# Kernel tuning notes

Hardware: AMD Instinct MI355X
Metric: run time of the kernel (lower is better)

Reference implementation:

```python
import jax, jax.numpy as jnp
import numpy as np

B, T, D, H, L, F = 256, 32, 1024, 8, 3, 2048
SSRC, NCOL, NTAB, NACT, NSYM = 64, 32, 16, 64, 32
HD = D // H


def setup_inputs() -> dict:
    key = jax.random.key(0)
    ks = jax.random.split(key, 40)
    n = lambda k, s, sc=0.02: jax.random.normal(k, s, jnp.float32) * sc
    inp = {}
    inp["prev_action_emb"] = jax.random.normal(ks[0], (B, T, D), jnp.float32)
    inp["encoded_src"] = jax.random.normal(ks[1], (B, SSRC, D), jnp.float32)
    inp["encoded_col"] = jax.random.normal(ks[2], (B, NCOL, D), jnp.float32)
    inp["encoded_tab"] = jax.random.normal(ks[3], (B, NTAB, D), jnp.float32)
    inp["src_mask"] = jnp.zeros((B, SSRC), jnp.int32)  # 1 = padded
    inp["symbol_ids"] = jax.random.randint(ks[4], (B, T), 0, NSYM)
    inp["view_type"] = jax.random.randint(ks[5], (B,), 0, 3)  # 0=action,1=col,2=tab
    inp["gold_action"] = jax.random.randint(ks[6], (B,), 0, NACT)
    inp["gold_col"] = jax.random.randint(ks[7], (B,), 0, NCOL)
    inp["gold_tab"] = jax.random.randint(ks[8], (B,), 0, NTAB)
    # grammar embeddings (torch nn.Embedding default ~ N(0,1))
    inp["symbol_emb"] = jax.random.normal(ks[9], (NSYM, D), jnp.float32)
    inp["action_emb"] = jax.random.normal(ks[10], (NACT, D), jnp.float32)
    # affine heads
    inp["action_aff_w"] = n(ks[11], (D, D)); inp["action_aff_b"] = jnp.zeros((D,), jnp.float32)
    inp["symbol_aff_w"] = n(ks[12], (D, D)); inp["symbol_aff_b"] = jnp.zeros((D,), jnp.float32)
    inp["col_aff_w"] = n(ks[13], (D, D)); inp["col_aff_b"] = jnp.zeros((D,), jnp.float32)
    inp["tab_aff_w"] = n(ks[14], (D, D)); inp["tab_aff_b"] = jnp.zeros((D,), jnp.float32)
    inp["tgt_lin_w"] = n(ks[15], (2 * D, D)); inp["tgt_lin_b"] = jnp.zeros((D,), jnp.float32)
    inp["out_lin_w"] = n(ks[16], (D, D)); inp["out_lin_b"] = jnp.zeros((D,), jnp.float32)
    # transformer decoder layers (q,k,v,o stacked on axis 1)
    inp["self_w"] = n(ks[17], (L, 4, D, D)); inp["self_b"] = jnp.zeros((L, 4, D), jnp.float32)
    inp["cross_w"] = n(ks[18], (L, 4, D, D)); inp["cross_b"] = jnp.zeros((L, 4, D), jnp.float32)
    inp["ffn_w1"] = n(ks[19], (L, D, F)); inp["ffn_b1"] = jnp.zeros((L, F), jnp.float32)
    inp["ffn_w2"] = n(ks[20], (L, F, D)); inp["ffn_b2"] = jnp.zeros((L, D), jnp.float32)
    inp["ln_g"] = jnp.ones((L, 3, D), jnp.float32); inp["ln_b"] = jnp.zeros((L, 3, D), jnp.float32)
    return inp


def _pe(t, d):
    pos = jnp.arange(t, dtype=jnp.float32)[:, None]
    div = jnp.exp(jnp.arange(0, d, 2, dtype=jnp.float32) * (-np.log(10000.0) / d))
    pe = jnp.zeros((t, d), jnp.float32)
    pe = pe.at[:, 0::2].set(jnp.sin(pos * div)).at[:, 1::2].set(jnp.cos(pos * div))
    return pe


def _ln(x, g, b, eps=1e-5):
    m = jnp.mean(x, -1, keepdims=True)
    v = jnp.mean((x - m) ** 2, -1, keepdims=True)
    return (x - m) / jnp.sqrt(v + eps) * g + b


def _mha(xq, xkv, w, b, pad=None):
    # w: [4, D, D] for q,k,v,o; pad: [B, Tk] bool key-padding mask
    q = (xq @ w[0] + b[0]).reshape(xq.shape[0], -1, H, HD)
    k = (xkv @ w[1] + b[1]).reshape(xkv.shape[0], -1, H, HD)
    v = (xkv @ w[2] + b[2]).reshape(xkv.shape[0], -1, H, HD)
    s = jnp.einsum("bqhd,bkhd->bhqk", q, k) / np.sqrt(HD).astype(np.float32)
    if pad is not None:
        s = jnp.where(pad[:, None, None, :], -1e9, s)
    a = jax.nn.softmax(s, -1)
    o = jnp.einsum("bhqk,bkhd->bqhd", a, v).reshape(xq.shape[0], -1, D)
    return o @ w[3] + b[3]


def reference(prev_action_emb, encoded_src, encoded_col, encoded_tab, symbol_emb, action_emb,
              action_aff_w, action_aff_b, symbol_aff_w, symbol_aff_b, col_aff_w, col_aff_b,
              tab_aff_w, tab_aff_b, tgt_lin_w, tgt_lin_b, out_lin_w, out_lin_b,
              self_w, self_b, cross_w, cross_b, ffn_w1, ffn_b1, ffn_w2, ffn_b2, ln_g, ln_b,
              src_mask, symbol_ids, view_type, gold_action, gold_col, gold_tab):
    # target embeddings: affine(prev action emb) ++ affine(symbol emb gather)
    tgt_a = prev_action_emb @ action_aff_w + action_aff_b            # [B,T,D]
    tgt_s = symbol_emb[symbol_ids] @ symbol_aff_w + symbol_aff_b     # [B,T,D]
    x = jnp.concatenate([tgt_a, tgt_s], -1) @ tgt_lin_w + tgt_lin_b  # [B,T,D]
    x = x + _pe(T, D)[None]  # positional encoding (dropout = eval identity)
    pad = src_mask.astype(bool)
    for l in range(L):  # post-LN TransformerDecoderLayer (torch default, relu FFN)
        x = _ln(x + _mha(x, x, self_w[l], self_b[l]), ln_g[l, 0], ln_b[l, 0])
        x = _ln(x + _mha(x, encoded_src, cross_w[l], cross_b[l], pad), ln_g[l, 1], ln_b[l, 1])
        ff = jax.nn.relu(x @ ffn_w1[l] + ffn_b1[l]) @ ffn_w2[l] + ffn_b2[l]
        x = _ln(x + ff, ln_g[l, 2], ln_b[l, 2])
    out = x[:, -1, :] @ out_lin_w + out_lin_b  # [B,D], last decode position
    # three routed prediction heads: affine(src) . out -> masked log_softmax
    src_a = action_emb @ action_aff_w + action_aff_b                 # [A,D]
    logp_a = jax.nn.log_softmax(out @ src_a.T, -1)                   # [B,A]
    src_c = encoded_col @ col_aff_w + col_aff_b                      # [B,Nc,D]
    logp_c = jax.nn.log_softmax(jnp.einsum("bnd,bd->bn", src_c, out), -1)
    src_t = encoded_tab @ tab_aff_w + tab_aff_b                      # [B,Nt,D]
    logp_t = jax.nn.log_softmax(jnp.einsum("bnd,bd->bn", src_t, out), -1)
    ga = jnp.take_along_axis(logp_a, gold_action[:, None], 1)[:, 0]
    gc = jnp.take_along_axis(logp_c, gold_col[:, None], 1)[:, 0]
    gt = jnp.take_along_axis(logp_t, gold_tab[:, None], 1)[:, 0]
    # grammar routing: each example's loss comes from exactly one view
    nll = -jnp.where(view_type == 0, ga, jnp.where(view_type == 1, gc, gt))  # [B]
    return nll
```

## Files before the change

kernel.cpp:

```cpp
#include <hip/hip_runtime.h>

typedef float  f32x4 __attribute__((ext_vector_type(4)));
typedef short  s16x8 __attribute__((ext_vector_type(8)));

__device__ __forceinline__ float b2f(short s) {
    return __uint_as_float(((unsigned)(unsigned short)s) << 16);
}
__device__ __forceinline__ short f2b(float f) {
    unsigned u = __float_as_uint(f);
    u = u + 0x7fffu + ((u >> 16) & 1u);
    return (short)(u >> 16);
}

__device__ __forceinline__ void gld_lds16(const short* g, short* l) {
    __builtin_amdgcn_global_load_lds(
        (const __attribute__((address_space(1))) unsigned int*)(const void*)g,
        (__attribute__((address_space(3))) unsigned int*)(void*)l,
        16, 0, 0);
}

#define S_VMCNT(N)  asm volatile("s_waitcnt vmcnt(" #N ")" ::: "memory")
#define S_LGKM0     asm volatile("s_waitcnt lgkmcnt(0)" ::: "memory")
#define SBAR        __builtin_amdgcn_s_barrier()
#define SCHED0      __builtin_amdgcn_sched_barrier(0)

template<int BM>
__global__ __launch_bounds__(512) void gemm_pipe(
    const short* __restrict__ A, const short* __restrict__ Bt,
    const float* __restrict__ bias,
    short* __restrict__ Cb,
    const short* __restrict__ res,
    const float* __restrict__ sym2, const int* __restrict__ sid,
    const float* __restrict__ pe,
    int M, int N, int K, int epi)
{
    constexpr int MF   = BM / 32;
    constexpr int ALW  = BM / 128;
    constexpr int BUFB = (BM + 256) * 64;
    __shared__ short lds[3 * BUFB / 2];

    const int tid  = threadIdx.x;
    const int lane = tid & 63;
    const int wave = tid >> 6;

    int bid = blockIdx.x;
    int nwg = gridDim.x;
    if ((nwg & 7) == 0) { int q = nwg >> 3; bid = (bid & 7) * q + (bid >> 3); }
    const int nbx = N >> 8;
    const int m0 = (bid / nbx) * BM;
    const int n0 = (bid % nbx) * 256;

    const int wm = (wave >> 2) * (BM / 2);
    const int wn = (wave & 3) * 64;
    const int l15 = lane & 15, l4 = lane >> 4;

    f32x4 acc[MF][4];
#pragma unroll
    for (int m = 0; m < MF; m++)
#pragma unroll
        for (int n = 0; n < 4; n++)
#pragma unroll
            for (int j = 0; j < 4; j++) acc[m][n][j] = 0.f;

    int aoff[MF], boff[4];
#pragma unroll
    for (int m = 0; m < MF; m++) {
        int r = wm + m * 16 + l15;
        aoff[m] = r * 64 + ((l4 ^ ((r >> 1) & 3)) << 4);
    }
#pragma unroll
    for (int n = 0; n < 4; n++) {
        int r = wn + n * 16 + l15;
        boff[n] = BM * 64 + r * 64 + ((l4 ^ ((r >> 1) & 3)) << 4);
    }

    size_t agoff[ALW]; int aldo[ALW];
#pragma unroll
    for (int i = 0; i < ALW; i++) {
        int rr = (wave * ALW + i) * 16 + (lane >> 2);
        int c  = (lane & 3) ^ ((rr >> 1) & 3);
        agoff[i] = (size_t)(m0 + rr) * K + c * 8;
        aldo[i]  = (wave * ALW + i) * 1024;
    }
    size_t bgoff[2]; int bldo[2];
#pragma unroll
    for (int i = 0; i < 2; i++) {
        int rr = (wave * 2 + i) * 16 + (lane >> 2);
        int c  = (lane & 3) ^ ((rr >> 1) & 3);
        bgoff[i] = (size_t)(n0 + rr) * K + c * 8;
        bldo[i]  = BM * 64 + (wave * 2 + i) * 1024;
    }

    char* lbase = (char*)lds;
    auto stage = [&](int kt, int bufoff) {
        char* lb = lbase + bufoff;
#pragma unroll
        for (int i = 0; i < ALW; i++)
            gld_lds16(A + agoff[i] + (size_t)kt * 32, (short*)(lb + aldo[i]));
#pragma unroll
        for (int i = 0; i < 2; i++)
            gld_lds16(Bt + bgoff[i] + (size_t)kt * 32, (short*)(lb + bldo[i]));
    };

    const int NT = K >> 5;
    stage(0, 0);
    stage(1, BUFB);
    if constexpr (BM == 256) S_VMCNT(4); else S_VMCNT(3);
    SBAR; SCHED0;

    int cbo = 0, sbo = 2 * BUFB;
    for (int t = 0; t < NT; t++) {
        if (t + 2 < NT) stage(t + 2, sbo);
        if constexpr (BM == 256) S_VMCNT(8); else S_VMCNT(6);
        SCHED0;
        s16x8 af[MF], bfv[4];
        const char* cp = lbase + cbo;
#pragma unroll
        for (int m = 0; m < MF; m++) af[m]  = *(const s16x8*)(cp + aoff[m]);
#pragma unroll
        for (int n = 0; n < 4; n++)  bfv[n] = *(const s16x8*)(cp + boff[n]);
        S_LGKM0;
        SCHED0;
        if constexpr (BM == 256) S_VMCNT(4); else S_VMCNT(3);
        SBAR; SCHED0;
        __builtin_amdgcn_s_setprio(1);
#pragma unroll
        for (int m = 0; m < MF; m++)
#pragma unroll
            for (int n = 0; n < 4; n++)
                acc[m][n] = __builtin_amdgcn_mfma_f32_16x16x32_bf16(
                    af[m], bfv[n], acc[m][n], 0, 0, 0);
        __builtin_amdgcn_s_setprio(0);
        cbo += BUFB; if (cbo == 3 * BUFB) cbo = 0;
        sbo += BUFB; if (sbo == 3 * BUFB) sbo = 0;
    }

#pragma unroll
    for (int m = 0; m < MF; m++) {
#pragma unroll
        for (int n = 0; n < 4; n++) {
#pragma unroll
            for (int j = 0; j < 4; j++) {
                int row = m0 + wm + m * 16 + l4 * 4 + j;
                int col = n0 + wn + n * 16 + l15;
                float v = acc[m][n][j];
                if (bias) v += bias[col];
                size_t idx = (size_t)row * N + col;
                if (epi == 0) {
                    Cb[idx] = f2b(v);
                } else if (epi == 2) {
                    v += sym2[(size_t)sid[row] * 1024 + col] + pe[(size_t)(row & 31) * 1024 + col];
                    Cb[idx] = f2b(v);
                } else if (epi == 3) {
                    Cb[idx] = f2b(fmaxf(v, 0.f));
                } else {
                    Cb[idx] = f2b(v + b2f(res[idx]));
                }
            }
        }
    }
}

__global__ __launch_bounds__(256) void gemm_bt(
    const short* __restrict__ A, const short* __restrict__ Bt,
    const float* __restrict__ bias,
    float* __restrict__ Cf, short* __restrict__ Cb,
    const short* __restrict__ res,
    int M, int N, int K, int epi)
{
    __shared__ short As[128 * 64];
    __shared__ short Bs[128 * 64];
    const int tid  = threadIdx.x;
    const int lane = tid & 63;
    const int wave = tid >> 6;
    const int m0 = blockIdx.y * 128, n0 = blockIdx.x * 128;
    const int wm = (wave >> 1) * 64, wn = (wave & 1) * 64;
    const int l15 = lane & 15, l4 = lane >> 4;

    f32x4 acc[4][4];
#pragma unroll
    for (int m = 0; m < 4; m++)
#pragma unroll
        for (int n = 0; n < 4; n++)
#pragma unroll
            for (int j = 0; j < 4; j++) acc[m][n][j] = 0.f;

    const int srow = wave * 32 + (lane >> 3);
    const int scol = (lane & 7) * 8;
    const short* Ag = A  + (size_t)(m0 + srow) * K + scol;
    const short* Bg = Bt + (size_t)(n0 + srow) * K + scol;
    short* Al = As + (wave * 32) * 64;
    short* Bl = Bs + (wave * 32) * 64;

    for (int k0 = 0; k0 < K; k0 += 64) {
#pragma unroll
        for (int i = 0; i < 4; i++) {
            gld_lds16(Ag + (size_t)(i * 8) * K + k0, Al + i * 8 * 64);
            gld_lds16(Bg + (size_t)(i * 8) * K + k0, Bl + i * 8 * 64);
        }
        __syncthreads();
#pragma unroll
        for (int kk = 0; kk < 64; kk += 32) {
            s16x8 af[4], bfv[4];
#pragma unroll
            for (int m = 0; m < 4; m++)
                af[m] = *(const s16x8*)(As + (wm + m * 16 + l15) * 64 + kk + l4 * 8);
#pragma unroll
            for (int n = 0; n < 4; n++)
                bfv[n] = *(const s16x8*)(Bs + (wn + n * 16 + l15) * 64 + kk + l4 * 8);
#pragma unroll
            for (int m = 0; m < 4; m++)
#pragma unroll
                for (int n = 0; n < 4; n++)
                    acc[m][n] = __builtin_amdgcn_mfma_f32_16x16x32_bf16(
                        af[m], bfv[n], acc[m][n], 0, 0, 0);
        }
        __syncthreads();
    }

#pragma unroll
    for (int m = 0; m < 4; m++) {
#pragma unroll
        for (int n = 0; n < 4; n++) {
#pragma unroll
            for (int j = 0; j < 4; j++) {
                int row = m0 + wm + m * 16 + l4 * 4 + j;
                int col = n0 + wn + n * 16 + l15;
                float v = acc[m][n][j];
                if (bias) v += bias[col];
                size_t idx = (size_t)row * N + col;
                if (epi == 0) {
                    Cb[idx] = f2b(v);
                } else if (epi == 1) {
                    Cf[idx] = v;
                } else if (epi == 3) {
                    Cb[idx] = f2b(fmaxf(v, 0.f));
                } else if (epi == 6) {
                    Cb[idx] = f2b(v + b2f(res[idx]));
                } else {
                    Cf[idx] = v; Cb[idx] = f2b(v);
                }
            }
        }
    }
}

__global__ __launch_bounds__(256) void attn_self(const short* __restrict__ qkv,
                                                 short* __restrict__ o)
{
    const int b = blockIdx.x >> 3, h = blockIdx.x & 7;
    __shared__ short Q[32 * 128], Kk[32 * 128], Vv[32 * 128];
    __shared__ float S[32 * 32];
    const int tid = threadIdx.x;
    const size_t base = (size_t)b * 32 * 3072 + h * 128;
    for (int i = tid; i < 512; i += 256) {
        int r = i >> 4, c = (i & 15) * 8;
        size_t g = base + (size_t)r * 3072 + c;
        *(s16x8*)(Q  + r * 128 + c) = *(const s16x8*)(qkv + g);
        *(s16x8*)(Kk + r * 128 + c) = *(const s16x8*)(qkv + g + 1024);
        *(s16x8*)(Vv + r * 128 + c) = *(const s16x8*)(qkv + g + 2048);
    }
    __syncthreads();
    for (int i = tid; i < 1024; i += 256) {
        int r = i >> 5, c = i & 31;
        float s = 0.f;
        for (int d8 = 0; d8 < 16; d8++) {
            s16x8 qa = *(const s16x8*)(Q  + r * 128 + d8 * 8);
            s16x8 ka = *(const s16x8*)(Kk + c * 128 + d8 * 8);
#pragma unroll
            for (int j = 0; j < 8; j++) s += b2f(qa[j]) * b2f(ka[j]);
        }
        S[i] = s * 0.088388347648318447f;
    }
    __syncthreads();
    if (tid < 32) {
        float mx = -1e30f;
        for (int c = 0; c < 32; c++) mx = fmaxf(mx, S[tid * 32 + c]);
        float sum = 0.f;
        for (int c = 0; c < 32; c++) { float p = __expf(S[tid * 32 + c] - mx); S[tid * 32 + c] = p; sum += p; }
        float inv = 1.f / sum;
        for (int c = 0; c < 32; c++) S[tid * 32 + c] *= inv;
    }
    __syncthreads();
    for (int i = tid; i < 4096; i += 256) {
        int r = i >> 7, d = i & 127;
        float a = 0.f;
        for (int c = 0; c < 32; c++) a += S[r * 32 + c] * b2f(Vv[c * 128 + d]);
        o[(size_t)(b * 32 + r) * 1024 + h * 128 + d] = f2b(a);
    }
}

__global__ __launch_bounds__(256) void attn_cross(const short* __restrict__ q_,
                                                  const short* __restrict__ ckv,
                                                  const int* __restrict__ mask,
                                                  short* __restrict__ o)
{
    const int b = blockIdx.x >> 3, h = blockIdx.x & 7;
    __shared__ short Q[32 * 128], Kk[64 * 128], Vv[64 * 128];
    __shared__ float S[32 * 64];
    const int tid = threadIdx.x;
    for (int i = tid; i < 512; i += 256) {
        int r = i >> 4, c = (i & 15) * 8;
        *(s16x8*)(Q + r * 128 + c) = *(const s16x8*)(q_ + (size_t)(b * 32 + r) * 1024 + h * 128 + c);
    }
    for (int i = tid; i < 1024; i += 256) {
        int r = i >> 4, c = (i & 15) * 8;
        size_t g = (size_t)(b * 64 + r) * 2048 + h * 128 + c;
        *(s16x8*)(Kk + r * 128 + c) = *(const s16x8*)(ckv + g);
        *(s16x8*)(Vv + r * 128 + c) = *(const s16x8*)(ckv + g + 1024);
    }
    __syncthreads();
    for (int i = tid; i < 2048; i += 256) {
        int r = i >> 6, c = i & 63;
        float s = 0.f;
        for (int d8 = 0; d8 < 16; d8++) {
            s16x8 qa = *(const s16x8*)(Q  + r * 128 + d8 * 8);
            s16x8 ka = *(const s16x8*)(Kk + c * 128 + d8 * 8);
#pragma unroll
            for (int j = 0; j < 8; j++) s += b2f(qa[j]) * b2f(ka[j]);
        }
        s *= 0.088388347648318447f;
        if (mask[b * 64 + c] != 0) s = -1e9f;
        S[i] = s;
    }
    __syncthreads();
    if (tid < 32) {
        float mx = -1e30f;
        for (int c = 0; c < 64; c++) mx = fmaxf(mx, S[tid * 64 + c]);
        float sum = 0.f;
        for (int c = 0; c < 64; c++) { float p = __expf(S[tid * 64 + c] - mx); S[tid * 64 + c] = p; sum += p; }
        float inv = 1.f / sum;
        for (int c = 0; c < 64; c++) S[tid * 64 + c] *= inv;
    }
    __syncthreads();
    for (int i = tid; i < 4096; i += 256) {
        int r = i >> 7, d = i & 127;
        float a = 0.f;
        for (int c = 0; c < 64; c++) a += S[r * 64 + c] * b2f(Vv[c * 128 + d]);
        o[(size_t)(b * 32 + r) * 1024 + h * 128 + d] = f2b(a);
    }
}

__global__ __launch_bounds__(256) void attn_self_last(const short* __restrict__ q,
                                                      const short* __restrict__ kv,
                                                      short* __restrict__ out)
{
    __shared__ float qs[4][128];
    __shared__ float ps[4][32];
    const int wave = threadIdx.x >> 6, lane = threadIdx.x & 63;
    const int idx = blockIdx.x * 4 + wave;
    const int b = idx >> 3, h = idx & 7;
    for (int d = lane; d < 128; d += 64)
        qs[wave][d] = b2f(q[(size_t)b * 1024 + h * 128 + d]);
    __syncthreads();
    float s = -1e30f;
    if (lane < 32) {
        const short* kr = kv + (size_t)(b * 32 + lane) * 2048 + h * 128;
        float a = 0.f;
        for (int d = 0; d < 128; d += 8) {
            s16x8 kvv = *(const s16x8*)(kr + d);
#pragma unroll
            for (int j = 0; j < 8; j++) a += qs[wave][d + j] * b2f(kvv[j]);
        }
        s = a * 0.088388347648318447f;
    }
    float mx = s;
#pragma unroll
    for (int o = 1; o < 32; o <<= 1) mx = fmaxf(mx, __shfl_xor(mx, o));
    float p = (lane < 32) ? __expf(s - mx) : 0.f;
    float sum = p;
#pragma unroll
    for (int o = 1; o < 32; o <<= 1) sum += __shfl_xor(sum, o);
    if (lane < 32) ps[wave][lane] = p / sum;
    __syncthreads();
    for (int d = lane; d < 128; d += 64) {
        float a = 0.f;
        for (int j = 0; j < 32; j++)
            a += ps[wave][j] * b2f(kv[(size_t)(b * 32 + j) * 2048 + 1024 + h * 128 + d]);
        out[(size_t)b * 1024 + h * 128 + d] = f2b(a);
    }
}

__global__ __launch_bounds__(256) void attn_cross_last(const short* __restrict__ q,
                                                       const short* __restrict__ ckv,
                                                       const int* __restrict__ mask,
                                                       short* __restrict__ out)
{
    __shared__ float qs[4][128];
    __shared__ float ps[4][64];
    const int wave = threadIdx.x >> 6, lane = threadIdx.x & 63;
    const int idx = blockIdx.x * 4 + wave;
    const int b = idx >> 3, h = idx & 7;
    for (int d = lane; d < 128; d += 64)
        qs[wave][d] = b2f(q[(size_t)b * 1024 + h * 128 + d]);
    __syncthreads();
    const short* kr = ckv + (size_t)(b * 64 + lane) * 2048 + h * 128;
    float a = 0.f;
    for (int d = 0; d < 128; d += 8) {
        s16x8 kvv = *(const s16x8*)(kr + d);
#pragma unroll
        for (int j = 0; j < 8; j++) a += qs[wave][d + j] * b2f(kvv[j]);
    }
    float s = a * 0.088388347648318447f;
    if (mask[b * 64 + lane] != 0) s = -1e9f;
    float mx = s;
#pragma unroll
    for (int o = 1; o < 64; o <<= 1) mx = fmaxf(mx, __shfl_xor(mx, o));
    float p = __expf(s - mx);
    float sum = p;
#pragma unroll
    for (int o = 1; o < 64; o <<= 1) sum += __shfl_xor(sum, o);
    ps[wave][lane] = p / sum;
    __syncthreads();
    for (int d = lane; d < 128; d += 64) {
        float acc = 0.f;
        for (int j = 0; j < 64; j++)
            acc += ps[wave][j] * b2f(ckv[(size_t)(b * 64 + j) * 2048 + 1024 + h * 128 + d]);
        out[(size_t)b * 1024 + h * 128 + d] = f2b(acc);
    }
}

__global__ __launch_bounds__(128) void ln_rows_b(const short* __restrict__ X,
                                                 short* __restrict__ Y,
                                                 const float* __restrict__ g,
                                                 const float* __restrict__ bt)
{
    const int row = blockIdx.x, tid = threadIdx.x;
    s16x8 v = *(const s16x8*)(X + (size_t)row * 1024 + tid * 8);
    float f[8];
    float s = 0.f, q = 0.f;
#pragma unroll
    for (int j = 0; j < 8; j++) { f[j] = b2f(v[j]); s += f[j]; q += f[j] * f[j]; }
#pragma unroll
    for (int o = 1; o < 64; o <<= 1) { s += __shfl_xor(s, o); q += __shfl_xor(q, o); }
    __shared__ float ls[2], lq[2];
    if ((tid & 63) == 0) { ls[tid >> 6] = s; lq[tid >> 6] = q; }
    __syncthreads();
    s = ls[0] + ls[1];
    q = lq[0] + lq[1];
    const float mean = s * 0.0009765625f;
    const float var  = q * 0.0009765625f - mean * mean;
    const float rs = rsqrtf(var + 1e-5f);
    s16x8 ov;
#pragma unroll
    for (int j = 0; j < 8; j++) {
        int c = tid * 8 + j;
        ov[j] = f2b((f[j] - mean) * rs * g[c] + bt[c]);
    }
    *(s16x8*)(Y + (size_t)row * 1024 + tid * 8) = ov;
}

__global__ __launch_bounds__(256) void convf2b(const float* __restrict__ s,
                                               short* __restrict__ d, int n)
{
    int i = (blockIdx.x * 256 + threadIdx.x) * 8;
    if (i < n) {
        float4 a = *(const float4*)(s + i);
        float4 b = *(const float4*)(s + i + 4);
        s16x8 o;
        o[0] = f2b(a.x); o[1] = f2b(a.y); o[2] = f2b(a.z); o[3] = f2b(a.w);
        o[4] = f2b(b.x); o[5] = f2b(b.y); o[6] = f2b(b.z); o[7] = f2b(b.w);
        *(s16x8*)(d + i) = o;
    }
}

__global__ __launch_bounds__(256) void transpose_conv_b(const float* __restrict__ src0,
                                                        short* __restrict__ dst0,
                                                        int R, int C)
{
    const float* src = src0 + (size_t)blockIdx.z * R * C;
    short* dst = dst0 + (size_t)blockIdx.z * R * C;
    __shared__ float t[32][33];
    int c0 = blockIdx.x * 32, r0 = blockIdx.y * 32;
    int tx = threadIdx.x & 31, ty = threadIdx.x >> 5;
#pragma unroll
    for (int i = 0; i < 32; i += 8) t[ty + i][tx] = src[(size_t)(r0 + ty + i) * C + c0 + tx];
    __syncthreads();
#pragma unroll
    for (int i = 0; i < 32; i += 8) dst[(size_t)(c0 + ty + i) * R + r0 + tx] = f2b(t[tx][ty + i]);
}

__global__ __launch_bounds__(256) void pad_conv(const float* __restrict__ s,
                                                short* __restrict__ d, int src_rows)
{
    int i = blockIdx.x * 256 + threadIdx.x;
    int r = i >> 10;
    d[i] = (r < src_rows) ? f2b(s[i]) : (short)0;
}

__global__ __launch_bounds__(256) void pe_build(float* __restrict__ pe)
{
    int i = blockIdx.x * 256 + threadIdx.x;
    int t = i >> 10, d = i & 1023;
    int de = d & ~1;
    float ang = (float)t * expf((float)de * (-9.2103403719761836f / 1024.f));
    pe[i] = (d & 1) ? cosf(ang) : sinf(ang);
}

__global__ __launch_bounds__(256) void gather_last(const short* __restrict__ x,
                                                   short* __restrict__ xlast)
{
    int i = blockIdx.x * 256 + threadIdx.x;
    int b = i >> 10, d = i & 1023;
    xlast[i] = x[((size_t)(b * 32 + 31) << 10) + d];
}

__global__ __launch_bounds__(64) void head_final(
    const float* __restrict__ logits_a,
    const float* __restrict__ enc_col_f, const short* __restrict__ yc,
    const float* __restrict__ enc_tab_f, const short* __restrict__ yt,
    const float* __restrict__ outf,
    const float* __restrict__ col_b, const float* __restrict__ tab_b,
    const int* __restrict__ view, const int* __restrict__ ga,
    const int* __restrict__ gc, const int* __restrict__ gt,
    float* __restrict__ nll)
{
    const int b = blockIdx.x, lane = threadIdx.x;
    const int vt = view[b];
    if (vt == 0) {
        float x = logits_a[(size_t)b * 128 + lane];
        float mx = x;
#pragma unroll
        for (int o = 1; o < 64; o <<= 1) mx = fmaxf(mx, __shfl_xor(mx, o));
        float sum = __expf(x - mx);
#pragma unroll
        for (int o = 1; o < 64; o <<= 1) sum += __shfl_xor(sum, o);
        float lse = mx + logf(sum);
        float gl = __shfl(x, ga[b]);
        if (lane == 0) nll[b] = lse - gl;
    } else {
        const int nit = (vt == 1) ? 32 : 16;
        const float* enc = (vt == 1) ? (enc_col_f + (size_t)b * 32 * 1024)
                                     : (enc_tab_f + (size_t)b * 16 * 1024);
        const short* y   = (vt == 1) ? (yc + (size_t)b * 1024) : (yt + (size_t)b * 1024);
        const float* bb  = (vt == 1) ? col_b : tab_b;
        float bc = 0.f;
        for (int i = lane; i < 1024; i += 64) bc += bb[i] * outf[(size_t)b * 1024 + i];
#pragma unroll
        for (int o = 1; o < 64; o <<= 1) bc += __shfl_xor(bc, o);
        float logit = -1e30f;
        if (lane < nit) {
            float s = bc;
            const float* er = enc + (size_t)lane * 1024;
            for (int d8 = 0; d8 < 128; d8++) {
                s16x8 yv = *(const s16x8*)(y + d8 * 8);
                float4 e0 = *(const float4*)(er + d8 * 8);
                float4 e1 = *(const float4*)(er + d8 * 8 + 4);
                s += e0.x * b2f(yv[0]) + e0.y * b2f(yv[1]) + e0.z * b2f(yv[2]) + e0.w * b2f(yv[3])
                   + e1.x * b2f(yv[4]) + e1.y * b2f(yv[5]) + e1.z * b2f(yv[6]) + e1.w * b2f(yv[7]);
            }
            logit = s;
        }
        float mx = logit;
#pragma unroll
        for (int o = 1; o < 64; o <<= 1) mx = fmaxf(mx, __shfl_xor(mx, o));
        float sum = (lane < nit) ? __expf(logit - mx) : 0.f;
#pragma unroll
        for (int o = 1; o < 64; o <<= 1) sum += __shfl_xor(sum, o);
        float lse = mx + logf(sum);
        int g = (vt == 1) ? gc[b] : gt[b];
        float gl = __shfl(logit, g);
        if (lane == 0) nll[b] = lse - gl;
    }
}

extern "C" void kernel_launch(void* const* d_in, const int* in_sizes, int n_in,
                              void* d_out, int out_size, void* d_ws, size_t ws_size,
                              hipStream_t stream)
{
    const float* pa_f     = (const float*)d_in[0];
    const float* src_f    = (const float*)d_in[1];
    const float* colenc_f = (const float*)d_in[2];
    const float* tabenc_f = (const float*)d_in[3];
    const int*   src_mask = (const int*)d_in[4];
    const int*   sym_ids  = (const int*)d_in[5];
    const int*   view     = (const int*)d_in[6];
    const int*   gold_a   = (const int*)d_in[7];
    const int*   gold_c   = (const int*)d_in[8];
    const int*   gold_t   = (const int*)d_in[9];
    const float* sym_emb  = (const float*)d_in[10];
    const float* act_emb  = (const float*)d_in[11];
    const float* Aaff_w   = (const float*)d_in[12];
    const float* Aaff_b   = (const float*)d_in[13];
    const float* Saff_w   = (const float*)d_in[14];
    const float* Saff_b   = (const float*)d_in[15];
    const float* Caff_w   = (const float*)d_in[16];
    const float* Caff_b   = (const float*)d_in[17];
    const float* Taff_w   = (const float*)d_in[18];
    const float* Taff_b   = (const float*)d_in[19];
    const float* tgt_w    = (const float*)d_in[20];
    const float* tgt_b    = (const float*)d_in[21];
    const float* outw     = (const float*)d_in[22];
    const float* outbias  = (const float*)d_in[23];
    const float* self_w   = (const float*)d_in[24];
    const float* self_b   = (const float*)d_in[25];
    const float* cross_w  = (const float*)d_in[26];
    const float* cross_b  = (const float*)d_in[27];
    const float* f1w      = (const float*)d_in[28];
    const float* f1b      = (const float*)d_in[29];
    const float* f2w      = (const float*)d_in[30];
    const float* f2bb     = (const float*)d_in[31];
    const float* lng      = (const float*)d_in[32];
    const float* lnbt     = (const float*)d_in[33];
    float* nll = (float*)d_out;

    char* ws = (char*)d_ws;
    size_t off = 0;
    auto alloc = [&](size_t bytes) -> char* {
        off = (off + 255) & ~(size_t)255;
        char* p = ws + off; off += bytes; return p;
    };

    const size_t MB1 = (size_t)1024 * 1024;
    short* WAaff  = (short*)alloc(MB1 * 2);
    short* WSaff  = (short*)alloc(MB1 * 2);
    short* Wtop   = (short*)alloc(MB1 * 2);
    short* Wbot   = (short*)alloc(MB1 * 2);
    short* Wout   = (short*)alloc(MB1 * 2);
    short* Wcol   = (short*)alloc(MB1 * 2);
    short* Wtab   = (short*)alloc(MB1 * 2);
    short* Wself  = (short*)alloc(12 * MB1 * 2);
    short* Wcross = (short*)alloc(12 * MB1 * 2);
    short* Wf1a   = (short*)alloc(3 * 2 * MB1 * 2);
    short* Wf2a   = (short*)alloc(3 * 2 * MB1 * 2);

    short* src_bf   = (short*)alloc((size_t)16384 * 1024 * 2);
    short* sym_pad  = (short*)alloc((size_t)128 * 1024 * 2);
    short* act_pad  = (short*)alloc((size_t)128 * 1024 * 2);
    short* sa_out   = (short*)alloc((size_t)128 * 1024 * 2);
    float* sym2     = (float*)alloc((size_t)128 * 1024 * 4);
    float* pe       = (float*)alloc((size_t)32 * 1024 * 4);
    short* tgt_a    = (short*)alloc((size_t)8192 * 1024 * 2);
    short* x_bf     = (short*)alloc((size_t)8192 * 1024 * 2);
    short* tmpb     = (short*)alloc((size_t)8192 * 1024 * 2);
    short* arena    = (short*)alloc((size_t)16384 * 2048 * 2);
    short* xlast    = (short*)alloc((size_t)256 * 1024 * 2);
    float* outf     = (float*)alloc((size_t)256 * 1024 * 4);
    short* outb16   = (short*)alloc((size_t)256 * 1024 * 2);
    short* srca     = (short*)alloc((size_t)128 * 1024 * 2);
    float* logits_a = (float*)alloc((size_t)256 * 128 * 4);
    short* ycb      = (short*)alloc((size_t)256 * 1024 * 2);
    short* ytb      = (short*)alloc((size_t)256 * 1024 * 2);
    short* xq31     = (short*)alloc((size_t)256 * 1024 * 2);
    short* x256a    = (short*)alloc((size_t)256 * 1024 * 2);
    short* x256b    = (short*)alloc((size_t)256 * 1024 * 2);
    short* q256     = (short*)alloc((size_t)256 * 1024 * 2);
    short* cq256    = (short*)alloc((size_t)256 * 1024 * 2);
    short* o256     = (short*)alloc((size_t)256 * 1024 * 2);
    short* h256     = (short*)alloc((size_t)256 * 2048 * 2);
    short* tmpb256  = (short*)alloc((size_t)256 * 1024 * 2);

    short* pa_bf = tmpb;
    short* cq    = tmpb;
    short* attn  = tgt_a;

    const dim3 BLK(256);
    auto conv = [&](const float* s, short* d, size_t n) {
        convf2b<<<dim3((unsigned)(n / 8 / 256)), BLK, 0, stream>>>(s, d, (int)n);
    };
    auto trans = [&](const float* s, short* d, int R, int C, int nm) {
        transpose_conv_b<<<dim3(C / 32, R / 32, nm), BLK, 0, stream>>>(s, d, R, C);
    };
    auto gp = [&](const short* A, const short* Bt, const float* bias,
                  short* Cb, const short* res,
                  const float* sy, const int* si, const float* pp,
                  int M, int N, int K, int epi, int BM) {
        if (BM == 256)
            gemm_pipe<256><<<dim3((N / 256) * (M / 256)), dim3(512), 0, stream>>>(
                A, Bt, bias, Cb, res, sy, si, pp, M, N, K, epi);
        else
            gemm_pipe<128><<<dim3((N / 256) * (M / 128)), dim3(512), 0, stream>>>(
                A, Bt, bias, Cb, res, sy, si, pp, M, N, K, epi);
    };
    auto gsm = [&](const short* A, const short* Bt, const float* bias,
                   float* Cf, short* Cb, const short* res,
                   int M, int N, int K, int epi) {
        gemm_bt<<<dim3(N / 128, M / 128), BLK, 0, stream>>>(
            A, Bt, bias, Cf, Cb, res, M, N, K, epi);
    };

    pe_build<<<dim3(128), BLK, 0, stream>>>(pe);
    conv(pa_f, pa_bf, (size_t)8192 * 1024);
    conv(src_f, src_bf, (size_t)16384 * 1024);
    conv(Caff_w, Wcol, MB1);
    conv(Taff_w, Wtab, MB1);
    pad_conv<<<dim3(512), BLK, 0, stream>>>(sym_emb, sym_pad, 32);
    pad_conv<<<dim3(512), BLK, 0, stream>>>(act_emb, act_pad, 64);
    trans(Aaff_w, WAaff, 1024, 1024, 1);
    trans(Saff_w, WSaff, 1024, 1024, 1);
    trans(tgt_w, Wtop, 1024, 1024, 1);
    trans(tgt_w + MB1, Wbot, 1024, 1024, 1);
    trans(outw, Wout, 1024, 1024, 1);
    trans(self_w, Wself, 1024, 1024, 12);
    trans(cross_w, Wcross, 1024, 1024, 12);
    trans(f1w, Wf1a, 1024, 2048, 3);
    trans(f2w, Wf2a, 2048, 1024, 3);

    gsm(sym_pad, WSaff, Saff_b, nullptr, sa_out, nullptr, 128, 1024, 1024, 0);
    gsm(sa_out, Wbot, nullptr, sym2, nullptr, nullptr, 128, 1024, 1024, 1);
    gp(pa_bf, WAaff, Aaff_b, tgt_a, nullptr, nullptr, nullptr, nullptr,
       8192, 1024, 1024, 0, 128);
    gp(tgt_a, Wtop, tgt_b, x_bf, nullptr, sym2, sym_ids, pe,
       8192, 1024, 1024, 2, 128);

    for (int l = 0; l < 2; l++) {
        const float* sb = self_b + (size_t)l * 4096;
        const float* cb = cross_b + (size_t)l * 4096;
        gp(x_bf, Wself + (size_t)(4 * l) * MB1, sb, arena, nullptr, nullptr, nullptr, nullptr,
           8192, 3072, 1024, 0, 256);
        attn_self<<<dim3(2048), BLK, 0, stream>>>(arena, attn);
        gp(attn, Wself + (size_t)(4 * l + 3) * MB1, sb + 3072, tmpb, x_bf, nullptr, nullptr, nullptr,
           8192, 1024, 1024, 6, 128);
        ln_rows_b<<<dim3(8192), dim3(128), 0, stream>>>(tmpb, x_bf,
            lng + (size_t)(l * 3 + 0) * 1024, lnbt + (size_t)(l * 3 + 0) * 1024);
        gp(x_bf, Wcross + (size_t)(4 * l) * MB1, cb, cq, nullptr, nullptr, nullptr, nullptr,
           8192, 1024, 1024, 0, 128);
        gp(src_bf, Wcross + (size_t)(4 * l + 1) * MB1, cb + 1024, arena, nullptr, nullptr, nullptr, nullptr,
           16384, 2048, 1024, 0, 256);
        attn_cross<<<dim3(2048), BLK, 0, stream>>>(cq, arena, src_mask, attn);
        gp(attn, Wcross + (size_t)(4 * l + 3) * MB1, cb + 3072, tmpb, x_bf, nullptr, nullptr, nullptr,
           8192, 1024, 1024, 6, 128);
        ln_rows_b<<<dim3(8192), dim3(128), 0, stream>>>(tmpb, x_bf,
            lng + (size_t)(l * 3 + 1) * 1024, lnbt + (size_t)(l * 3 + 1) * 1024);
        gp(x_bf, Wf1a + (size_t)l * 2 * MB1, f1b + (size_t)l * 2048, arena, nullptr, nullptr, nullptr, nullptr,
           8192, 2048, 1024, 3, 256);
        gp(arena, Wf2a + (size_t)l * 2 * MB1, f2bb + (size_t)l * 1024, tmpb, x_bf, nullptr, nullptr, nullptr,
           8192, 1024, 2048, 6, 128);
        ln_rows_b<<<dim3(8192), dim3(128), 0, stream>>>(tmpb, x_bf,
            lng + (size_t)(l * 3 + 2) * 1024, lnbt + (size_t)(l * 3 + 2) * 1024);
    }

    {
        const float* sb = self_b + (size_t)2 * 4096;
        const float* cb = cross_b + (size_t)2 * 4096;
        gather_last<<<dim3(1024), BLK, 0, stream>>>(x_bf, xq31);
        gp(x_bf, Wself + (size_t)(4 * 2 + 1) * MB1, sb + 1024, arena, nullptr, nullptr, nullptr, nullptr,
           8192, 2048, 1024, 0, 256);
        gsm(xq31, Wself + (size_t)(4 * 2) * MB1, sb, nullptr, q256, nullptr, 256, 1024, 1024, 0);
        attn_self_last<<<dim3(512), BLK, 0, stream>>>(q256, arena, o256);
        gsm(o256, Wself + (size_t)(4 * 2 + 3) * MB1, sb + 3072, nullptr, tmpb256, xq31, 256, 1024, 1024, 6);
        ln_rows_b<<<dim3(256), dim3(128), 0, stream>>>(tmpb256, x256a,
            lng + (size_t)(2 * 3 + 0) * 1024, lnbt + (size_t)(2 * 3 + 0) * 1024);
        gsm(x256a, Wcross + (size_t)(4 * 2) * MB1, cb, nullptr, cq256, nullptr, 256, 1024, 1024, 0);
        gp(src_bf, Wcross + (size_t)(4 * 2 + 1) * MB1, cb + 1024, arena, nullptr, nullptr, nullptr, nullptr,
           16384, 2048, 1024, 0, 256);
        attn_cross_last<<<dim3(512), BLK, 0, stream>>>(cq256, arena, src_mask, o256);
        gsm(o256, Wcross + (size_t)(4 * 2 + 3) * MB1, cb + 3072, nullptr, tmpb256, x256a, 256, 1024, 1024, 6);
        ln_rows_b<<<dim3(256), dim3(128), 0, stream>>>(tmpb256, x256b,
            lng + (size_t)(2 * 3 + 1) * 1024, lnbt + (size_t)(2 * 3 + 1) * 1024);
        gsm(x256b, Wf1a + (size_t)2 * 2 * MB1, f1b + (size_t)2 * 2048, nullptr, h256, nullptr,
            256, 2048, 1024, 3);
        gsm(h256, Wf2a + (size_t)2 * 2 * MB1, f2bb + (size_t)2 * 1024, nullptr, tmpb256, x256b,
            256, 1024, 2048, 6);
        ln_rows_b<<<dim3(256), dim3(128), 0, stream>>>(tmpb256, xlast,
            lng + (size_t)(2 * 3 + 2) * 1024, lnbt + (size_t)(2 * 3 + 2) * 1024);
    }

    gsm(xlast, Wout, outbias, outf, outb16, nullptr, 256, 1024, 1024, 5);
    gsm(act_pad, WAaff, Aaff_b, nullptr, srca, nullptr, 128, 1024, 1024, 0);
    gsm(outb16, srca, nullptr, logits_a, nullptr, nullptr, 256, 128, 1024, 1);
    gsm(outb16, Wcol, nullptr, nullptr, ycb, nullptr, 256, 1024, 1024, 0);
    gsm(outb16, Wtab, nullptr, nullptr, ytb, nullptr, 256, 1024, 1024, 0);
    head_final<<<dim3(256), dim3(64), 0, stream>>>(
        logits_a, colenc_f, ycb, tabenc_f, ytb, outf,
        Caff_b, Taff_b, view, gold_a, gold_c, gold_t, nll);
}
```

Before: 2.551 ms.

## Switch GEMM to BK=64 double-buffered pipeline with 8-way XOR swizzle

Restructures the bf16 MFMA GEMM main loop from a three-stage BK=32 ring to a two-stage BK=64 double buffer, doing two MFMA sub-steps per K tile and one barrier per 64-wide K step. The LDS layout uses 128-byte rows with an 8-chunk XOR swizzle keyed on the lane, and the global-to-LDS load mapping is changed to match. This halves the loop iterations and barriers, at the cost of a shallower prefetch depth and a full vmcnt(0) wait each iteration, which may expose global load latency.

```diff
diff --git a/kernel.cpp b/kernel.cpp
--- a/kernel.cpp
+++ b/kernel.cpp
@@ -19,7 +19,7 @@
         16, 0, 0);
 }
 
-#define S_VMCNT(N)  asm volatile("s_waitcnt vmcnt(" #N ")" ::: "memory")
+#define S_VMCNT0    asm volatile("s_waitcnt vmcnt(0)" ::: "memory")
 #define S_LGKM0     asm volatile("s_waitcnt lgkmcnt(0)" ::: "memory")
 #define SBAR        __builtin_amdgcn_s_barrier()
 #define SCHED0      __builtin_amdgcn_sched_barrier(0)
@@ -35,9 +35,9 @@
     int M, int N, int K, int epi)
 {
     constexpr int MF   = BM / 32;
-    constexpr int ALW  = BM / 128;
-    constexpr int BUFB = (BM + 256) * 64;
-    __shared__ short lds[3 * BUFB / 2];
+    constexpr int ALW  = BM / 64;
+    constexpr int BUFB = (BM + 256) * 128;
+    __shared__ short lds[2 * (BM + 256) * 64];
 
     const int tid  = threadIdx.x;
     const int lane = tid & 63;
@@ -53,6 +53,7 @@
     const int wm = (wave >> 2) * (BM / 2);
     const int wn = (wave & 3) * 64;
     const int l15 = lane & 15, l4 = lane >> 4;
+    const int key = lane & 7;
 
     f32x4 acc[MF][4];
 #pragma unroll
@@ -66,73 +67,85 @@
 #pragma unroll
     for (int m = 0; m < MF; m++) {
         int r = wm + m * 16 + l15;
-        aoff[m] = r * 64 + ((l4 ^ ((r >> 1) & 3)) << 4);
+        aoff[m] = r * 128 + ((l4 ^ key) << 4);
     }
 #pragma unroll
     for (int n = 0; n < 4; n++) {
         int r = wn + n * 16 + l15;
-        boff[n] = BM * 64 + r * 64 + ((l4 ^ ((r >> 1) & 3)) << 4);
-    }
-
+        boff[n] = BM * 128 + r * 128 + ((l4 ^ key) << 4);
+    }
+
+    const int lrow = lane >> 3;
+    const int lchunk = (lane & 7) ^ lrow;
     size_t agoff[ALW]; int aldo[ALW];
 #pragma unroll
     for (int i = 0; i < ALW; i++) {
-        int rr = (wave * ALW + i) * 16 + (lane >> 2);
-        int c  = (lane & 3) ^ ((rr >> 1) & 3);
-        agoff[i] = (size_t)(m0 + rr) * K + c * 8;
-        aldo[i]  = (wave * ALW + i) * 1024;
-    }
-    size_t bgoff[2]; int bldo[2];
-#pragma unroll
-    for (int i = 0; i < 2; i++) {
-        int rr = (wave * 2 + i) * 16 + (lane >> 2);
-        int c  = (lane & 3) ^ ((rr >> 1) & 3);
-        bgoff[i] = (size_t)(n0 + rr) * K + c * 8;
-        bldo[i]  = BM * 64 + (wave * 2 + i) * 1024;
+        int rr = wave * (BM / 8) + i * 8;
+        agoff[i] = (size_t)(m0 + rr + lrow) * K + lchunk * 8;
+        aldo[i]  = rr * 128;
+    }
+    size_t bgoff[4]; int bldo[4];
+#pragma unroll
+    for (int i = 0; i < 4; i++) {
+        int rr = wave * 32 + i * 8;
+        bgoff[i] = (size_t)(n0 + rr + lrow) * K + lchunk * 8;
+        bldo[i]  = BM * 128 + rr * 128;
     }
 
     char* lbase = (char*)lds;
     auto stage = [&](int kt, int bufoff) {
         char* lb = lbase + bufoff;
+        const size_t ke = (size_t)kt * 64;
 #pragma unroll
         for (int i = 0; i < ALW; i++)
-            gld_lds16(A + agoff[i] + (size_t)kt * 32, (short*)(lb + aldo[i]));
-#pragma unroll
-        for (int i = 0; i < 2; i++)
-            gld_lds16(Bt + bgoff[i] + (size_t)kt * 32, (short*)(lb + bldo[i]));
+            gld_lds16(A + agoff[i] + ke, (short*)(lb + aldo[i]));
+#pragma unroll
+        for (int i = 0; i < 4; i++)
+            gld_lds16(Bt + bgoff[i] + ke, (short*)(lb + bldo[i]));
     };
 
-    const int NT = K >> 5;
+    const int NT = K >> 6;
     stage(0, 0);
-    stage(1, BUFB);
-    if constexpr (BM == 256) S_VMCNT(4); else S_VMCNT(3);
-    SBAR; SCHED0;
-
-    int cbo = 0, sbo = 2 * BUFB;
+    S_VMCNT0; SCHED0; SBAR; SCHED0;
+
+    int cb = 0;
     for (int t = 0; t < NT; t++) {
-        if (t + 2 < NT) stage(t + 2, sbo);
-        if constexpr (BM == 256) S_VMCNT(8); else S_VMCNT(6);
-        SCHED0;
-        s16x8 af[MF], bfv[4];
-        const char* cp = lbase + cbo;
-#pragma unroll
-        for (int m = 0; m < MF; m++) af[m]  = *(const s16x8*)(cp + aoff[m]);
-#pragma unroll
-        for (int n = 0; n < 4; n++)  bfv[n] = *(const s16x8*)(cp + boff[n]);
-        S_LGKM0;
-        SCHED0;
-        if constexpr (BM == 256) S_VMCNT(4); else S_VMCNT(3);
-        SBAR; SCHED0;
-        __builtin_amdgcn_s_setprio(1);
-#pragma unroll
-        for (int m = 0; m < MF; m++)
-#pragma unroll
-            for (int n = 0; n < 4; n++)
-                acc[m][n] = __builtin_amdgcn_mfma_f32_16x16x32_bf16(
-                    af[m], bfv[n], acc[m][n], 0, 0, 0);
-        __builtin_amdgcn_s_setprio(0);
-        cbo += BUFB; if (cbo == 3 * BUFB) cbo = 0;
-        sbo += BUFB; if (sbo == 3 * BUFB) sbo = 0;
+        if (t + 1 < NT) stage(t + 1, (cb ^ 1) * BUFB);
+        const char* cp = lbase + cb * BUFB;
+        {
+            s16x8 af[MF], bv[4];
+#pragma unroll
+            for (int m = 0; m < MF; m++) af[m] = *(const s16x8*)(cp + aoff[m]);
+#pragma unroll
+            for (int n = 0; n < 4; n++)  bv[n] = *(const s16x8*)(cp + boff[n]);
+            S_LGKM0; SCHED0;
+            __builtin_amdgcn_s_setprio(1);
+#pragma unroll
+            for (int m = 0; m < MF; m++)
+#pragma unroll
+                for (int n = 0; n < 4; n++)
+                    acc[m][n] = __builtin_amdgcn_mfma_f32_16x16x32_bf16(
+                        af[m], bv[n], acc[m][n], 0, 0, 0);
+            __builtin_amdgcn_s_setprio(0);
+        }
+        {
+            s16x8 af[MF], bv[4];
+#pragma unroll
+            for (int m = 0; m < MF; m++) af[m] = *(const s16x8*)(cp + (aoff[m] ^ 64));
+#pragma unroll
+            for (int n = 0; n < 4; n++)  bv[n] = *(const s16x8*)(cp + (boff[n] ^ 64));
+            S_LGKM0; SCHED0;
+            __builtin_amdgcn_s_setprio(1);
+#pragma unroll
+            for (int m = 0; m < MF; m++)
+#pragma unroll
+                for (int n = 0; n < 4; n++)
+                    acc[m][n] = __builtin_amdgcn_mfma_f32_16x16x32_bf16(
+                        af[m], bv[n], acc[m][n], 0, 0, 0);
+            __builtin_amdgcn_s_setprio(0);
+        }
+        S_VMCNT0; SCHED0; SBAR; SCHED0;
+        cb ^= 1;
     }
 
 #pragma unroll
```

Result: no change. 2.521 ms (-1.2%).

## Deepen GEMM LDS pipeline to four buffers with three tiles in flight

Applied to the files above, without the earlier changes.

The bf16 GEMM kernel moves from a triple-buffered LDS ring with two K-tiles prefetched to a four-slot ring with three tiles prefetched. The vmcnt waits are rewritten to count down at the tail of the loop, and the barrier is placed before the LDS reads instead of between reads and MFMAs. Staging addresses are simplified, with a lane-based swizzle replacing the per-row swizzle computation. The aim is to hide more global-load latency behind the MFMAs, at the cost of more LDS per block (possibly lower occupancy) and a second barrier in each iteration.

```diff
diff --git a/kernel.cpp b/kernel.cpp
--- a/kernel.cpp
+++ b/kernel.cpp
@@ -37,7 +37,7 @@
     constexpr int MF   = BM / 32;
     constexpr int ALW  = BM / 128;
     constexpr int BUFB = (BM + 256) * 64;
-    __shared__ short lds[3 * BUFB / 2];
+    __shared__ short lds[4 * (BM + 256) * 32];
 
     const int tid  = threadIdx.x;
     const int lane = tid & 63;
@@ -74,65 +74,62 @@
         boff[n] = BM * 64 + r * 64 + ((l4 ^ ((r >> 1) & 3)) << 4);
     }
 
+    const int lrow = lane >> 2;
+    const int lch  = (lane & 3) ^ ((lane >> 3) & 3);
     size_t agoff[ALW]; int aldo[ALW];
 #pragma unroll
     for (int i = 0; i < ALW; i++) {
-        int rr = (wave * ALW + i) * 16 + (lane >> 2);
-        int c  = (lane & 3) ^ ((rr >> 1) & 3);
-        agoff[i] = (size_t)(m0 + rr) * K + c * 8;
-        aldo[i]  = (wave * ALW + i) * 1024;
+        int ar = wave * (BM / 8) + i * 16;
+        agoff[i] = (size_t)(m0 + ar + lrow) * K + lch * 8;
+        aldo[i]  = ar * 64;
     }
     size_t bgoff[2]; int bldo[2];
 #pragma unroll
     for (int i = 0; i < 2; i++) {
-        int rr = (wave * 2 + i) * 16 + (lane >> 2);
-        int c  = (lane & 3) ^ ((rr >> 1) & 3);
-        bgoff[i] = (size_t)(n0 + rr) * K + c * 8;
-        bldo[i]  = BM * 64 + (wave * 2 + i) * 1024;
+        int br = wave * 32 + i * 16;
+        bgoff[i] = (size_t)(n0 + br + lrow) * K + lch * 8;
+        bldo[i]  = BM * 64 + br * 64;
     }
 
     char* lbase = (char*)lds;
-    auto stage = [&](int kt, int bufoff) {
-        char* lb = lbase + bufoff;
+    auto stage = [&](int kt) {
+        char* lb = lbase + (kt & 3) * BUFB;
+        const size_t ke = (size_t)kt * 32;
 #pragma unroll
         for (int i = 0; i < ALW; i++)
-            gld_lds16(A + agoff[i] + (size_t)kt * 32, (short*)(lb + aldo[i]));
+            gld_lds16(A + agoff[i] + ke, (short*)(lb + aldo[i]));
 #pragma unroll
         for (int i = 0; i < 2; i++)
-            gld_lds16(Bt + bgoff[i] + (size_t)kt * 32, (short*)(lb + bldo[i]));
+            gld_lds16(Bt + bgoff[i] + ke, (short*)(lb + bldo[i]));
     };
 
     const int NT = K >> 5;
-    stage(0, 0);
-    stage(1, BUFB);
-    if constexpr (BM == 256) S_VMCNT(4); else S_VMCNT(3);
-    SBAR; SCHED0;
-
-    int cbo = 0, sbo = 2 * BUFB;
+    stage(0); stage(1); stage(2);
+
     for (int t = 0; t < NT; t++) {
-        if (t + 2 < NT) stage(t + 2, sbo);
-        if constexpr (BM == 256) S_VMCNT(8); else S_VMCNT(6);
-        SCHED0;
-        s16x8 af[MF], bfv[4];
-        const char* cp = lbase + cbo;
-#pragma unroll
-        for (int m = 0; m < MF; m++) af[m]  = *(const s16x8*)(cp + aoff[m]);
-#pragma unroll
-        for (int n = 0; n < 4; n++)  bfv[n] = *(const s16x8*)(cp + boff[n]);
-        S_LGKM0;
-        SCHED0;
-        if constexpr (BM == 256) S_VMCNT(4); else S_VMCNT(3);
-        SBAR; SCHED0;
+        if (t + 3 < NT) stage(t + 3);
+        const int rem = NT - 1 - t;
+        if (rem >= 3)      { if constexpr (ALW == 2) S_VMCNT(12); else S_VMCNT(9); }
+        else if (rem == 2) { if constexpr (ALW == 2) S_VMCNT(8);  else S_VMCNT(6); }
+        else if (rem == 1) { if constexpr (ALW == 2) S_VMCNT(4);  else S_VMCNT(3); }
+        else               S_VMCNT(0);
+        SCHED0; SBAR; SCHED0;
+
+        const char* cp = lbase + (t & 3) * BUFB;
+        s16x8 af[MF], bv[4];
+#pragma unroll
+        for (int m = 0; m < MF; m++) af[m] = *(const s16x8*)(cp + aoff[m]);
+#pragma unroll
+        for (int n = 0; n < 4; n++)  bv[n] = *(const s16x8*)(cp + boff[n]);
         __builtin_amdgcn_s_setprio(1);
 #pragma unroll
         for (int m = 0; m < MF; m++)
 #pragma unroll
             for (int n = 0; n < 4; n++)
                 acc[m][n] = __builtin_amdgcn_mfma_f32_16x16x32_bf16(
-                    af[m], bfv[n], acc[m][n], 0, 0, 0);
+                    af[m], bv[n], acc[m][n], 0, 0, 0);
         __builtin_amdgcn_s_setprio(0);
-        cbo += BUFB; if (cbo == 3 * BUFB) cbo = 0;
-        sbo += BUFB; if (sbo == 3 * BUFB) sbo = 0;
+        S_LGKM0; SCHED0; SBAR; SCHED0;
     }
 
 #pragma unroll
```

New measurement: 2.647 ms. +3.8%, slower.
